# Kernel optimization log

Hardware: AMD Instinct MI355X
Metric: run time of the kernel (lower is better)

Reference implementation:

```python
import jax, jax.numpy as jnp
import numpy as np

HEADS, DIM_HEAD, DIM = 8, 64, 512
INNER = HEADS * DIM_HEAD  # 512


def setup_inputs() -> dict:
    key = jax.random.key(0)
    k1, k2, k3 = jax.random.split(key, 3)
    b, n = 2, 2048
    x = jax.random.normal(k1, (b, n, DIM), dtype=jnp.float32)
    # to_qkv: Linear(dim, 4*inner_dim, bias=False); weight stored [out, in]
    w_qkv = jax.random.normal(k2, (4 * INNER, DIM), dtype=jnp.float32) * (1.0 / np.sqrt(DIM))
    # to_out: Linear(2*inner_dim, dim) with bias
    w_out = jax.random.normal(k3, (DIM, 2 * INNER), dtype=jnp.float32) * (1.0 / np.sqrt(2 * INNER))
    b_out = jnp.zeros((DIM,), dtype=jnp.float32)
    return {"x": x, "w_qkv": w_qkv, "w_out": w_out, "b_out": b_out}


def reference(x, w_qkv, w_out, b_out):
    b, n, d = x.shape
    qkvt = x @ w_qkv.T  # [b, n, 4*inner]
    q, k, v, t = jnp.split(qkvt, 4, axis=-1)

    def split_heads(z):
        return z.reshape(b, n, HEADS, DIM_HEAD).transpose(0, 2, 1, 3)  # [b,h,n,dh]

    q, k, v, t = map(split_heads, (q, k, v, t))

    scale = DIM_HEAD ** -0.5
    dots = jnp.einsum('bhid,bhjd->bhij', q, k) * scale
    attn1 = jax.nn.softmax(dots, axis=-1)

    # fixed positional-decay attention: exp(-|i-j|/e), torch broadcast-normalized
    idx = jnp.arange(1, n + 1, dtype=x.dtype)  # linspace(1, n, n)
    tg = jnp.abs(idx[None, :] - idx[:, None])  # [n, n]
    a2 = jnp.exp(-tg / jnp.exp(jnp.asarray(1.0, x.dtype)))
    a2 = a2 / a2.sum(-1)  # broadcasts over last axis, as in the torch code

    out1 = jnp.einsum('bhij,bhjd->bhid', attn1, v)
    out2 = jnp.einsum('ij,bhjd->bhid', a2, t)
    out = jnp.concatenate([out1, out2], axis=-1)  # [b,h,n,2*dh]
    out = out.transpose(0, 2, 1, 3).reshape(b, n, HEADS * 2 * DIM_HEAD)  # [b,n,2*inner]
    return out @ w_out.T + b_out
```

## Files before the change

### kernel.cpp

```cpp
#include <hip/hip_runtime.h>
#include <stdint.h>

typedef unsigned short u16;
typedef __bf16 bf16;
typedef __bf16 bf16x8 __attribute__((ext_vector_type(8)));
typedef float f32x4 __attribute__((ext_vector_type(4)));

#define NSEQ 2048
#define NDH 64
#define NH 8
#define QKS 2097152ull

__device__ __forceinline__ float b2f(u16 u) {
  union { float f; uint32_t i; } x; x.i = ((uint32_t)u) << 16; return x.f;
}
__device__ __forceinline__ u16 f2b(float f) {
  union { float f; uint32_t i; } x; x.f = f;
  const uint32_t r = x.i + 0x7FFFu + ((x.i >> 16) & 1u);
  return (u16)(r >> 16);
}

__global__ __launch_bounds__(256) void k_cvt(
    const float* __restrict__ x, const float* __restrict__ wqkv,
    const float* __restrict__ wout, u16* __restrict__ xbf,
    u16* __restrict__ wqkvbf, u16* __restrict__ woutbf) {
  const int i = blockIdx.x * 256 + threadIdx.x;
  const float* src; u16* dst; int off;
  if (i < 524288)      { src = x;    dst = xbf;    off = i; }
  else if (i < 786432) { src = wqkv; dst = wqkvbf; off = i - 524288; }
  else                 { src = wout; dst = woutbf; off = i - 786432; }
  const float4 v = *(const float4*)(src + (size_t)off * 4);
  u16 t[4] = {f2b(v.x), f2b(v.y), f2b(v.z), f2b(v.w)};
  *(uint2*)(dst + (size_t)off * 4) = *(const uint2*)t;
}

__global__ __launch_bounds__(256) void k_gemm_qkvt(
    const u16* __restrict__ X, const u16* __restrict__ W, u16* __restrict__ qkvt) {
  __shared__ __align__(16) bf16 smem[18432];
  bf16* As = smem;
  bf16* Bs = smem + 5120;
  const int tid = threadIdx.x;
  const int n0 = blockIdx.x * 128;
  const int m0 = blockIdx.y * 128;
  const int w = tid >> 6, lane = tid & 63;
  const int wy = w >> 1, wx = w & 1;
  const int quad = lane >> 4, l15 = lane & 15;
  const int srow = tid >> 1, shalf = (tid & 1) * 16;
  const u16* ax = X + (size_t)(m0 + srow) * 512 + shalf;
  const u16* bx = W + (size_t)(n0 + srow) * 512 + shalf;
  f32x4 acc[4][4];
#pragma unroll
  for (int mt = 0; mt < 4; ++mt)
#pragma unroll
    for (int nt = 0; nt < 4; ++nt) acc[mt][nt] = (f32x4){0.f, 0.f, 0.f, 0.f};
  uint4 a0 = *(const uint4*)ax, a1 = *(const uint4*)(ax + 8);
  uint4 b0 = *(const uint4*)bx, b1 = *(const uint4*)(bx + 8);
  for (int kc = 0; kc < 512; kc += 32) {
    __syncthreads();
    *(uint4*)&As[srow * 40 + shalf]     = a0;
    *(uint4*)&As[srow * 40 + shalf + 8] = a1;
    *(uint4*)&Bs[srow * 40 + shalf]     = b0;
    *(uint4*)&Bs[srow * 40 + shalf + 8] = b1;
    __syncthreads();
    if (kc + 32 < 512) {
      a0 = *(const uint4*)(ax + kc + 32);
      a1 = *(const uint4*)(ax + kc + 40);
      b0 = *(const uint4*)(bx + kc + 32);
      b1 = *(const uint4*)(bx + kc + 40);
    }
    bf16x8 af[4], bfr[4];
#pragma unroll
    for (int mt = 0; mt < 4; ++mt)
      af[mt] = *(const bf16x8*)&As[(wy * 64 + mt * 16 + l15) * 40 + quad * 8];
#pragma unroll
    for (int nt = 0; nt < 4; ++nt)
      bfr[nt] = *(const bf16x8*)&Bs[(wx * 64 + nt * 16 + l15) * 40 + quad * 8];
#pragma unroll
    for (int mt = 0; mt < 4; ++mt)
#pragma unroll
      for (int nt = 0; nt < 4; ++nt)
        acc[mt][nt] = __builtin_amdgcn_mfma_f32_16x16x32_bf16(af[mt], bfr[nt], acc[mt][nt], 0, 0, 0);
  }
  __syncthreads();
  const int cbase = n0 + wx * 64;
  const int which = cbase >> 9;
  const int h     = (cbase >> 6) & 7;
  const float scale = (which == 0) ? 0.18033688011112043f : 1.0f;
  bf16* Cw = smem + w * 4608;
  if (which == 2) {
#pragma unroll
    for (int nt = 0; nt < 4; ++nt)
#pragma unroll
      for (int mt = 0; mt < 4; ++mt)
#pragma unroll
        for (int r = 0; r < 4; ++r)
          Cw[(nt * 16 + l15) * 72 + mt * 16 + quad * 4 + r] = (bf16)acc[mt][nt][r];
  } else {
#pragma unroll
    for (int mt = 0; mt < 4; ++mt)
#pragma unroll
      for (int nt = 0; nt < 4; ++nt)
#pragma unroll
        for (int r = 0; r < 4; ++r)
          Cw[(mt * 16 + quad * 4 + r) * 72 + nt * 16 + l15] = (bf16)(acc[mt][nt][r] * scale);
  }
  const int mb = m0 + wy * 64;
  const int bb = mb >> 11;
  const int nn0 = mb & (NSEQ - 1);
  if (which == 2) {
    u16* vt = qkvt + 2ull * QKS + (size_t)(bb * NH + h) * NDH * NSEQ;
#pragma unroll
    for (int p = 0; p < 8; ++p) {
      const int d = p * 8 + (lane >> 3);
      const int t8 = (lane & 7) * 8;
      const uint4 v = *(const uint4*)&Cw[d * 72 + t8];
      *(uint4*)(vt + (size_t)d * NSEQ + nn0 + t8) = v;
    }
  } else {
    u16* dst = qkvt + (size_t)which * QKS + ((size_t)(bb * NH + h) * NSEQ + nn0) * NDH;
#pragma unroll
    for (int p = 0; p < 8; ++p) {
      const int tok = p * 8 + (lane >> 3);
      const int c8 = (lane & 7) * 8;
      const uint4 v = *(const uint4*)&Cw[tok * 72 + c8];
      *(uint4*)(dst + (size_t)tok * NDH + c8) = v;
    }
  }
}

__global__ __launch_bounds__(256) void k_attn(
    const u16* __restrict__ qkvt, u16* __restrict__ out12) {
  __shared__ __align__(16) bf16 Qs[64][72];
  __shared__ __align__(16) bf16 Ks[64][72];
  __shared__ __align__(16) bf16 Vt[64][72];
  __shared__ __align__(16) bf16 Pw[64][72];
  const int tid = threadIdx.x;
  const int q0  = blockIdx.x * 64;
  const int bh  = blockIdx.y;
  const size_t base  = (size_t)bh * (NSEQ * NDH);
  const size_t vbase = 2ull * QKS + (size_t)bh * (NDH * NSEQ);
  const int wq = tid >> 6, lane = tid & 63;
  const int quad = lane >> 4, l15 = lane & 15;
  const int srow = tid >> 2, sc0 = (tid & 3) * 16;
  {
    const u16* qp = qkvt + base + (size_t)(q0 + srow) * NDH + sc0;
    *(uint4*)&Qs[srow][sc0]     = *(const uint4*)qp;
    *(uint4*)&Qs[srow][sc0 + 8] = *(const uint4*)(qp + 8);
  }
  __syncthreads();
  const bf16x8 qa0 = *(const bf16x8*)&Qs[wq * 16 + l15][quad * 8];
  const bf16x8 qa1 = *(const bf16x8*)&Qs[wq * 16 + l15][32 + quad * 8];
  bf16x8 vones;
#pragma unroll
  for (int j = 0; j < 8; ++j) vones[j] = (l15 == 0) ? (bf16)1.f : (bf16)0.f;
  f32x4 lacc = {0.f, 0.f, 0.f, 0.f};
  f32x4 o[4] = {{0.f,0.f,0.f,0.f},{0.f,0.f,0.f,0.f},{0.f,0.f,0.f,0.f},{0.f,0.f,0.f,0.f}};
  const u16* kp = qkvt + QKS + base + (size_t)srow * NDH + sc0;
  const u16* vp = qkvt + vbase + (size_t)srow * NSEQ + sc0;
  uint4 k0 = *(const uint4*)kp;
  uint4 k1 = *(const uint4*)(kp + 8);
  uint4 v0 = *(const uint4*)vp;
  uint4 v1 = *(const uint4*)(vp + 8);
  for (int kt = 0; kt < 32; ++kt) {
    __syncthreads();
    *(uint4*)&Ks[srow][sc0]     = k0;
    *(uint4*)&Ks[srow][sc0 + 8] = k1;
    *(uint4*)&Vt[srow][sc0]     = v0;
    *(uint4*)&Vt[srow][sc0 + 8] = v1;
    __syncthreads();
    if (kt < 31) {
      const u16* kn = kp + (size_t)(kt + 1) * 64 * NDH;
      const u16* vn = vp + (kt + 1) * 64;
      k0 = *(const uint4*)kn;
      k1 = *(const uint4*)(kn + 8);
      v0 = *(const uint4*)vn;
      v1 = *(const uint4*)(vn + 8);
    }
    f32x4 s[4] = {{0.f,0.f,0.f,0.f},{0.f,0.f,0.f,0.f},{0.f,0.f,0.f,0.f},{0.f,0.f,0.f,0.f}};
#pragma unroll
    for (int t = 0; t < 4; ++t) {
      const bf16x8 kb0 = *(const bf16x8*)&Ks[t * 16 + l15][quad * 8];
      const bf16x8 kb1 = *(const bf16x8*)&Ks[t * 16 + l15][32 + quad * 8];
      s[t] = __builtin_amdgcn_mfma_f32_16x16x32_bf16(qa0, kb0, s[t], 0, 0, 0);
      s[t] = __builtin_amdgcn_mfma_f32_16x16x32_bf16(qa1, kb1, s[t], 0, 0, 0);
    }
#pragma unroll
    for (int r = 0; r < 4; ++r) {
      const int prow = wq * 16 + quad * 4 + r;
      Pw[prow][l15]      = (bf16)__builtin_amdgcn_exp2f(s[0][r]);
      Pw[prow][16 + l15] = (bf16)__builtin_amdgcn_exp2f(s[1][r]);
      Pw[prow][32 + l15] = (bf16)__builtin_amdgcn_exp2f(s[2][r]);
      Pw[prow][48 + l15] = (bf16)__builtin_amdgcn_exp2f(s[3][r]);
    }
#pragma unroll
    for (int c = 0; c < 2; ++c) {
      const bf16x8 pa = *(const bf16x8*)&Pw[wq * 16 + l15][c * 32 + quad * 8];
      lacc = __builtin_amdgcn_mfma_f32_16x16x32_bf16(pa, vones, lacc, 0, 0, 0);
#pragma unroll
      for (int nt = 0; nt < 4; ++nt) {
        const bf16x8 vb = *(const bf16x8*)&Vt[nt * 16 + l15][c * 32 + quad * 8];
        o[nt] = __builtin_amdgcn_mfma_f32_16x16x32_bf16(pa, vb, o[nt], 0, 0, 0);
      }
    }
  }
  const int bb = bh >> 3, h = bh & 7;
#pragma unroll
  for (int r = 0; r < 4; ++r) {
    const float lsum = __shfl(lacc[r], lane & 48);
    const float inv = 1.f / lsum;
    const int nn = q0 + wq * 16 + quad * 4 + r;
    u16* dst = out12 + (size_t)(bb * NSEQ + nn) * 1024 + h * 128;
#pragma unroll
    for (int nt = 0; nt < 4; ++nt)
      dst[nt * 16 + l15] = f2b(o[nt][r] * inv);
  }
}

__global__ __launch_bounds__(256) void k_band(
    const u16* __restrict__ qkvt, u16* __restrict__ out12) {
  __shared__ float sinv[4][192];
  __shared__ float fbuf[4][64][68];
  const int tid = threadIdx.x;
  const int w = tid >> 6, d = tid & 63;
  const int c  = blockIdx.x * 4 + w;
  const int i0 = c * 64;
  const int bh = blockIdx.y;
  const size_t tb = 3ull * QKS + (size_t)bh * (NSEQ * NDH);
  const float EI = 0.36787944117144233f;
  const float RR = 0.69220062755534635f;
  const float OMR = 1.f - RR;
#pragma unroll
  for (int p = 0; p < 3; ++p) {
    const int j = i0 - 64 + p * 64 + d;
    const float r1 = __expf(-(float)(j + 1) * EI);
    const float r2 = __expf(-(float)(NSEQ - j) * EI);
    sinv[w][p * 64 + d] = OMR / (1.f - r1 + RR - r2);
  }
  const u16* tp = qkvt + tb + d;
  float f = 0.f;
  if (c > 0) {
#pragma unroll 8
    for (int jj = 0; jj < 64; ++jj)
      f = RR * f + sinv[w][jj] * b2f(tp[(size_t)(i0 - 64 + jj) * NDH]);
  }
#pragma unroll 8
  for (int jj = 0; jj < 64; ++jj) {
    f = RR * f + sinv[w][64 + jj] * b2f(tp[(size_t)(i0 + jj) * NDH]);
    fbuf[w][jj][d] = f;
  }
  float b = 0.f;
  if (c < 31) {
#pragma unroll 8
    for (int jj = 63; jj >= 0; --jj)
      b = RR * b + sinv[w][128 + jj] * b2f(tp[(size_t)(i0 + 64 + jj) * NDH]);
  }
  const int bb = bh >> 3, h = bh & 7;
#pragma unroll 8
  for (int jj = 63; jj >= 0; --jj) {
    const float g = sinv[w][64 + jj] * b2f(tp[(size_t)(i0 + jj) * NDH]);
    b = RR * b + g;
    out12[(size_t)(bb * NSEQ + i0 + jj) * 1024 + h * 128 + 64 + d] =
        f2b(fbuf[w][jj][d] + b - g);
  }
}

__global__ __launch_bounds__(256) void k_gemm_out(
    const u16* __restrict__ A, const u16* __restrict__ W,
    const float* __restrict__ bias, float* __restrict__ out) {
  __shared__ __align__(16) float smemf[8704];
  bf16* As = (bf16*)smemf;
  bf16* Bs = (bf16*)smemf + 5120;
  const int tid = threadIdx.x;
  const int n0 = blockIdx.x * 64;
  const int m0 = blockIdx.y * 128;
  const int w = tid >> 6, lane = tid & 63;
  const int quad = lane >> 4, l15 = lane & 15;
  const int srow = tid >> 1, shalf = (tid & 1) * 16;
  const u16* ap = A + (size_t)(m0 + srow) * 1024 + shalf;
  const int brow = (tid & 127) >> 1;
  const u16* bp = W + (size_t)(n0 + brow) * 1024 + shalf;
  f32x4 acc[2][4];
#pragma unroll
  for (int mt = 0; mt < 2; ++mt)
#pragma unroll
    for (int nt = 0; nt < 4; ++nt) acc[mt][nt] = (f32x4){0.f, 0.f, 0.f, 0.f};
  uint4 a0 = *(const uint4*)ap, a1 = *(const uint4*)(ap + 8);
  uint4 b0 = {}, b1 = {};
  if (tid < 128) { b0 = *(const uint4*)bp; b1 = *(const uint4*)(bp + 8); }
  for (int kc = 0; kc < 1024; kc += 32) {
    __syncthreads();
    *(uint4*)&As[srow * 40 + shalf]     = a0;
    *(uint4*)&As[srow * 40 + shalf + 8] = a1;
    if (tid < 128) {
      *(uint4*)&Bs[brow * 40 + shalf]     = b0;
      *(uint4*)&Bs[brow * 40 + shalf + 8] = b1;
    }
    __syncthreads();
    if (kc + 32 < 1024) {
      a0 = *(const uint4*)(ap + kc + 32);
      a1 = *(const uint4*)(ap + kc + 40);
      if (tid < 128) {
        b0 = *(const uint4*)(bp + kc + 32);
        b1 = *(const uint4*)(bp + kc + 40);
      }
    }
    bf16x8 af[2], bfr[4];
#pragma unroll
    for (int mt = 0; mt < 2; ++mt)
      af[mt] = *(const bf16x8*)&As[(w * 32 + mt * 16 + l15) * 40 + quad * 8];
#pragma unroll
    for (int nt = 0; nt < 4; ++nt)
      bfr[nt] = *(const bf16x8*)&Bs[(nt * 16 + l15) * 40 + quad * 8];
#pragma unroll
    for (int mt = 0; mt < 2; ++mt)
#pragma unroll
      for (int nt = 0; nt < 4; ++nt)
        acc[mt][nt] = __builtin_amdgcn_mfma_f32_16x16x32_bf16(af[mt], bfr[nt], acc[mt][nt], 0, 0, 0);
  }
  float bias_v[4];
#pragma unroll
  for (int nt = 0; nt < 4; ++nt) bias_v[nt] = bias[n0 + nt * 16 + l15];
  __syncthreads();
  float* Cw = smemf + w * 2176;
#pragma unroll
  for (int mt = 0; mt < 2; ++mt)
#pragma unroll
    for (int nt = 0; nt < 4; ++nt)
#pragma unroll
      for (int r = 0; r < 4; ++r)
        Cw[(mt * 16 + quad * 4 + r) * 68 + nt * 16 + l15] = acc[mt][nt][r] + bias_v[nt];
#pragma unroll
  for (int p = 0; p < 8; ++p) {
    const int row = p * 4 + (lane >> 4);
    const int c4  = lane & 15;
    const float4 v = *(const float4*)&Cw[row * 68 + c4 * 4];
    *(float4*)(out + (size_t)(m0 + w * 32 + row) * 512 + n0 + c4 * 4) = v;
  }
}

extern "C" void kernel_launch(void* const* d_in, const int* in_sizes, int n_in,
                              void* d_out, int out_size, void* d_ws, size_t ws_size,
                              hipStream_t stream) {
  (void)in_sizes; (void)n_in; (void)out_size; (void)ws_size;
  const float* x     = (const float*)d_in[0];
  const float* w_qkv = (const float*)d_in[1];
  const float* w_out = (const float*)d_in[2];
  const float* b_out = (const float*)d_in[3];
  float* out = (float*)d_out;
  u16* qkvt    = (u16*)d_ws;
  u16* out12   = (u16*)d_ws + 8ull * 1024 * 1024;
  u16* xbf     = out12;
  u16* wqkvbf  = (u16*)d_ws + 10ull * 1024 * 1024;
  u16* woutbf  = (u16*)d_ws + 12ull * 1024 * 1024;
  k_cvt      <<<3584, 256, 0, stream>>>(x, w_qkv, w_out, xbf, wqkvbf, woutbf);
  k_gemm_qkvt<<<dim3(16, 32), 256, 0, stream>>>(xbf, wqkvbf, qkvt);
  k_attn     <<<dim3(32, 16), 256, 0, stream>>>(qkvt, out12);
  k_band     <<<dim3(8, 16), 256, 0, stream>>>(qkvt, out12);
  k_gemm_out <<<dim3(8, 32), 256, 0, stream>>>(out12, woutbf, b_out, out);
}
```

Before: 158.1 us.

## Process 128 query rows per attention block to reuse K/V tiles

Each attention block now handles 128 queries instead of 64, with every wave owning 32 rows, so each K/V tile loaded into shared memory feeds twice as many MFMAs. The grid is halved to 256 blocks and reordered so blockIdx.x indexes batch-head. The P buffer row stride is padded to 76 to change the LDS bank pattern. This cuts global and LDS traffic per query, at the cost of more registers per thread and fewer blocks to spread across the GPU's compute units.

```diff
diff --git a/kernel.cpp b/kernel.cpp
--- a/kernel.cpp
+++ b/kernel.cpp
@@ -130,13 +130,13 @@
 
 __global__ __launch_bounds__(256) void k_attn(
     const u16* __restrict__ qkvt, u16* __restrict__ out12) {
-  __shared__ __align__(16) bf16 Qs[64][72];
+  __shared__ __align__(16) bf16 Qs[128][72];
   __shared__ __align__(16) bf16 Ks[64][72];
   __shared__ __align__(16) bf16 Vt[64][72];
-  __shared__ __align__(16) bf16 Pw[64][72];
+  __shared__ __align__(16) bf16 Pw[128][76];
   const int tid = threadIdx.x;
-  const int q0  = blockIdx.x * 64;
-  const int bh  = blockIdx.y;
+  const int bh  = blockIdx.x;
+  const int q0  = blockIdx.y * 128;
   const size_t base  = (size_t)bh * (NSEQ * NDH);
   const size_t vbase = 2ull * QKS + (size_t)bh * (NDH * NSEQ);
   const int wq = tid >> 6, lane = tid & 63;
@@ -146,15 +146,26 @@
     const u16* qp = qkvt + base + (size_t)(q0 + srow) * NDH + sc0;
     *(uint4*)&Qs[srow][sc0]     = *(const uint4*)qp;
     *(uint4*)&Qs[srow][sc0 + 8] = *(const uint4*)(qp + 8);
+    const u16* qp2 = qp + 64 * NDH;
+    *(uint4*)&Qs[64 + srow][sc0]     = *(const uint4*)qp2;
+    *(uint4*)&Qs[64 + srow][sc0 + 8] = *(const uint4*)(qp2 + 8);
   }
   __syncthreads();
-  const bf16x8 qa0 = *(const bf16x8*)&Qs[wq * 16 + l15][quad * 8];
-  const bf16x8 qa1 = *(const bf16x8*)&Qs[wq * 16 + l15][32 + quad * 8];
+  bf16x8 qa[2][2];
+#pragma unroll
+  for (int i = 0; i < 2; ++i)
+#pragma unroll
+    for (int c = 0; c < 2; ++c)
+      qa[i][c] = *(const bf16x8*)&Qs[wq * 32 + i * 16 + l15][c * 32 + quad * 8];
   bf16x8 vones;
 #pragma unroll
   for (int j = 0; j < 8; ++j) vones[j] = (l15 == 0) ? (bf16)1.f : (bf16)0.f;
-  f32x4 lacc = {0.f, 0.f, 0.f, 0.f};
-  f32x4 o[4] = {{0.f,0.f,0.f,0.f},{0.f,0.f,0.f,0.f},{0.f,0.f,0.f,0.f},{0.f,0.f,0.f,0.f}};
+  f32x4 lacc[2] = {{0.f,0.f,0.f,0.f},{0.f,0.f,0.f,0.f}};
+  f32x4 o[2][4];
+#pragma unroll
+  for (int i = 0; i < 2; ++i)
+#pragma unroll
+    for (int nt = 0; nt < 4; ++nt) o[i][nt] = (f32x4){0.f,0.f,0.f,0.f};
   const u16* kp = qkvt + QKS + base + (size_t)srow * NDH + sc0;
   const u16* vp = qkvt + vbase + (size_t)srow * NSEQ + sc0;
   uint4 k0 = *(const uint4*)kp;
@@ -176,44 +187,61 @@
       v0 = *(const uint4*)vn;
       v1 = *(const uint4*)(vn + 8);
     }
-    f32x4 s[4] = {{0.f,0.f,0.f,0.f},{0.f,0.f,0.f,0.f},{0.f,0.f,0.f,0.f},{0.f,0.f,0.f,0.f}};
+    f32x4 s[2][4];
+#pragma unroll
+    for (int i = 0; i < 2; ++i)
+#pragma unroll
+      for (int t = 0; t < 4; ++t) s[i][t] = (f32x4){0.f,0.f,0.f,0.f};
 #pragma unroll
     for (int t = 0; t < 4; ++t) {
       const bf16x8 kb0 = *(const bf16x8*)&Ks[t * 16 + l15][quad * 8];
       const bf16x8 kb1 = *(const bf16x8*)&Ks[t * 16 + l15][32 + quad * 8];
-      s[t] = __builtin_amdgcn_mfma_f32_16x16x32_bf16(qa0, kb0, s[t], 0, 0, 0);
-      s[t] = __builtin_amdgcn_mfma_f32_16x16x32_bf16(qa1, kb1, s[t], 0, 0, 0);
-    }
-#pragma unroll
-    for (int r = 0; r < 4; ++r) {
-      const int prow = wq * 16 + quad * 4 + r;
-      Pw[prow][l15]      = (bf16)__builtin_amdgcn_exp2f(s[0][r]);
-      Pw[prow][16 + l15] = (bf16)__builtin_amdgcn_exp2f(s[1][r]);
-      Pw[prow][32 + l15] = (bf16)__builtin_amdgcn_exp2f(s[2][r]);
-      Pw[prow][48 + l15] = (bf16)__builtin_amdgcn_exp2f(s[3][r]);
-    }
+#pragma unroll
+      for (int i = 0; i < 2; ++i) {
+        s[i][t] = __builtin_amdgcn_mfma_f32_16x16x32_bf16(qa[i][0], kb0, s[i][t], 0, 0, 0);
+        s[i][t] = __builtin_amdgcn_mfma_f32_16x16x32_bf16(qa[i][1], kb1, s[i][t], 0, 0, 0);
+      }
+    }
+#pragma unroll
+    for (int i = 0; i < 2; ++i)
+#pragma unroll
+      for (int r = 0; r < 4; ++r) {
+        const int prow = wq * 32 + i * 16 + quad * 4 + r;
+        Pw[prow][l15]      = (bf16)__builtin_amdgcn_exp2f(s[i][0][r]);
+        Pw[prow][16 + l15] = (bf16)__builtin_amdgcn_exp2f(s[i][1][r]);
+        Pw[prow][32 + l15] = (bf16)__builtin_amdgcn_exp2f(s[i][2][r]);
+        Pw[prow][48 + l15] = (bf16)__builtin_amdgcn_exp2f(s[i][3][r]);
+      }
 #pragma unroll
     for (int c = 0; c < 2; ++c) {
-      const bf16x8 pa = *(const bf16x8*)&Pw[wq * 16 + l15][c * 32 + quad * 8];
-      lacc = __builtin_amdgcn_mfma_f32_16x16x32_bf16(pa, vones, lacc, 0, 0, 0);
+      bf16x8 pa[2];
+#pragma unroll
+      for (int i = 0; i < 2; ++i) {
+        pa[i] = *(const bf16x8*)&Pw[wq * 32 + i * 16 + l15][c * 32 + quad * 8];
+        lacc[i] = __builtin_amdgcn_mfma_f32_16x16x32_bf16(pa[i], vones, lacc[i], 0, 0, 0);
+      }
 #pragma unroll
       for (int nt = 0; nt < 4; ++nt) {
         const bf16x8 vb = *(const bf16x8*)&Vt[nt * 16 + l15][c * 32 + quad * 8];
-        o[nt] = __builtin_amdgcn_mfma_f32_16x16x32_bf16(pa, vb, o[nt], 0, 0, 0);
+#pragma unroll
+        for (int i = 0; i < 2; ++i)
+          o[i][nt] = __builtin_amdgcn_mfma_f32_16x16x32_bf16(pa[i], vb, o[i][nt], 0, 0, 0);
       }
     }
   }
   const int bb = bh >> 3, h = bh & 7;
 #pragma unroll
-  for (int r = 0; r < 4; ++r) {
-    const float lsum = __shfl(lacc[r], lane & 48);
-    const float inv = 1.f / lsum;
-    const int nn = q0 + wq * 16 + quad * 4 + r;
-    u16* dst = out12 + (size_t)(bb * NSEQ + nn) * 1024 + h * 128;
-#pragma unroll
-    for (int nt = 0; nt < 4; ++nt)
-      dst[nt * 16 + l15] = f2b(o[nt][r] * inv);
-  }
+  for (int i = 0; i < 2; ++i)
+#pragma unroll
+    for (int r = 0; r < 4; ++r) {
+      const float lsum = __shfl(lacc[i][r], lane & 48);
+      const float inv = 1.f / lsum;
+      const int nn = q0 + wq * 32 + i * 16 + quad * 4 + r;
+      u16* dst = out12 + (size_t)(bb * NSEQ + nn) * 1024 + h * 128;
+#pragma unroll
+      for (int nt = 0; nt < 4; ++nt)
+        dst[nt * 16 + l15] = f2b(o[i][nt][r] * inv);
+    }
 }
 
 __global__ __launch_bounds__(256) void k_band(
@@ -354,7 +382,7 @@
   u16* woutbf  = (u16*)d_ws + 12ull * 1024 * 1024;
   k_cvt      <<<3584, 256, 0, stream>>>(x, w_qkv, w_out, xbf, wqkvbf, woutbf);
   k_gemm_qkvt<<<dim3(16, 32), 256, 0, stream>>>(xbf, wqkvbf, qkvt);
-  k_attn     <<<dim3(32, 16), 256, 0, stream>>>(qkvt, out12);
+  k_attn     <<<dim3(16, 16), 256, 0, stream>>>(qkvt, out12);
   k_band     <<<dim3(8, 16), 256, 0, stream>>>(qkvt, out12);
   k_gemm_out <<<dim3(8, 32), 256, 0, stream>>>(out12, woutbf, b_out, out);
 }
```

Result: slower. 163.5 us (+3.4%).

## Fuse fp32-to-bf16 conversion into GEMM loads and retile output GEMM

Applied to the files above, without the earlier changes.

Removes the standalone conversion kernel: the QKV and output GEMMs now read fp32 inputs and weights directly and convert to bf16 while staging into shared memory. This saves one launch and a round trip of bf16 copies through memory, but the GEMMs now read twice the bytes and redo the weight conversion in every block. The output GEMM moves to 64x64 tiles, doubling the block count. The attention grid swaps its axes so consecutive blocks share a head, and the P tile row stride is padded from 72 to 76.

```diff
diff --git a/kernel.cpp b/kernel.cpp
--- a/kernel.cpp
+++ b/kernel.cpp
@@ -20,22 +20,8 @@
   return (u16)(r >> 16);
 }
 
-__global__ __launch_bounds__(256) void k_cvt(
-    const float* __restrict__ x, const float* __restrict__ wqkv,
-    const float* __restrict__ wout, u16* __restrict__ xbf,
-    u16* __restrict__ wqkvbf, u16* __restrict__ woutbf) {
-  const int i = blockIdx.x * 256 + threadIdx.x;
-  const float* src; u16* dst; int off;
-  if (i < 524288)      { src = x;    dst = xbf;    off = i; }
-  else if (i < 786432) { src = wqkv; dst = wqkvbf; off = i - 524288; }
-  else                 { src = wout; dst = woutbf; off = i - 786432; }
-  const float4 v = *(const float4*)(src + (size_t)off * 4);
-  u16 t[4] = {f2b(v.x), f2b(v.y), f2b(v.z), f2b(v.w)};
-  *(uint2*)(dst + (size_t)off * 4) = *(const uint2*)t;
-}
-
 __global__ __launch_bounds__(256) void k_gemm_qkvt(
-    const u16* __restrict__ X, const u16* __restrict__ W, u16* __restrict__ qkvt) {
+    const float* __restrict__ X, const float* __restrict__ W, u16* __restrict__ qkvt) {
   __shared__ __align__(16) bf16 smem[18432];
   bf16* As = smem;
   bf16* Bs = smem + 5120;
@@ -46,32 +32,47 @@
   const int wy = w >> 1, wx = w & 1;
   const int quad = lane >> 4, l15 = lane & 15;
   const int srow = tid >> 1, shalf = (tid & 1) * 16;
-  const u16* ax = X + (size_t)(m0 + srow) * 512 + shalf;
-  const u16* bx = W + (size_t)(n0 + srow) * 512 + shalf;
+  const float* ax = X + (size_t)(m0 + srow) * 512 + shalf;
+  const float* bx = W + (size_t)(n0 + srow) * 512 + shalf;
   f32x4 acc[4][4];
 #pragma unroll
   for (int mt = 0; mt < 4; ++mt)
 #pragma unroll
     for (int nt = 0; nt < 4; ++nt) acc[mt][nt] = (f32x4){0.f, 0.f, 0.f, 0.f};
-  uint4 a0 = *(const uint4*)ax, a1 = *(const uint4*)(ax + 8);
-  uint4 b0 = *(const uint4*)bx, b1 = *(const uint4*)(bx + 8);
+  float4 af[4], bf4[4];
+#pragma unroll
+  for (int p = 0; p < 4; ++p) {
+    af[p]  = *(const float4*)(ax + p * 4);
+    bf4[p] = *(const float4*)(bx + p * 4);
+  }
   for (int kc = 0; kc < 512; kc += 32) {
     __syncthreads();
-    *(uint4*)&As[srow * 40 + shalf]     = a0;
-    *(uint4*)&As[srow * 40 + shalf + 8] = a1;
-    *(uint4*)&Bs[srow * 40 + shalf]     = b0;
-    *(uint4*)&Bs[srow * 40 + shalf + 8] = b1;
+    {
+      u16 ta[8] = {f2b(af[0].x), f2b(af[0].y), f2b(af[0].z), f2b(af[0].w),
+                   f2b(af[1].x), f2b(af[1].y), f2b(af[1].z), f2b(af[1].w)};
+      u16 tb[8] = {f2b(af[2].x), f2b(af[2].y), f2b(af[2].z), f2b(af[2].w),
+                   f2b(af[3].x), f2b(af[3].y), f2b(af[3].z), f2b(af[3].w)};
+      *(uint4*)&As[srow * 40 + shalf]     = *(const uint4*)ta;
+      *(uint4*)&As[srow * 40 + shalf + 8] = *(const uint4*)tb;
+      u16 tc[8] = {f2b(bf4[0].x), f2b(bf4[0].y), f2b(bf4[0].z), f2b(bf4[0].w),
+                   f2b(bf4[1].x), f2b(bf4[1].y), f2b(bf4[1].z), f2b(bf4[1].w)};
+      u16 td[8] = {f2b(bf4[2].x), f2b(bf4[2].y), f2b(bf4[2].z), f2b(bf4[2].w),
+                   f2b(bf4[3].x), f2b(bf4[3].y), f2b(bf4[3].z), f2b(bf4[3].w)};
+      *(uint4*)&Bs[srow * 40 + shalf]     = *(const uint4*)tc;
+      *(uint4*)&Bs[srow * 40 + shalf + 8] = *(const uint4*)td;
+    }
     __syncthreads();
     if (kc + 32 < 512) {
-      a0 = *(const uint4*)(ax + kc + 32);
-      a1 = *(const uint4*)(ax + kc + 40);
-      b0 = *(const uint4*)(bx + kc + 32);
-      b1 = *(const uint4*)(bx + kc + 40);
-    }
-    bf16x8 af[4], bfr[4];
+#pragma unroll
+      for (int p = 0; p < 4; ++p) {
+        af[p]  = *(const float4*)(ax + kc + 32 + p * 4);
+        bf4[p] = *(const float4*)(bx + kc + 32 + p * 4);
+      }
+    }
+    bf16x8 afr[4], bfr[4];
 #pragma unroll
     for (int mt = 0; mt < 4; ++mt)
-      af[mt] = *(const bf16x8*)&As[(wy * 64 + mt * 16 + l15) * 40 + quad * 8];
+      afr[mt] = *(const bf16x8*)&As[(wy * 64 + mt * 16 + l15) * 40 + quad * 8];
 #pragma unroll
     for (int nt = 0; nt < 4; ++nt)
       bfr[nt] = *(const bf16x8*)&Bs[(wx * 64 + nt * 16 + l15) * 40 + quad * 8];
@@ -79,7 +80,7 @@
     for (int mt = 0; mt < 4; ++mt)
 #pragma unroll
       for (int nt = 0; nt < 4; ++nt)
-        acc[mt][nt] = __builtin_amdgcn_mfma_f32_16x16x32_bf16(af[mt], bfr[nt], acc[mt][nt], 0, 0, 0);
+        acc[mt][nt] = __builtin_amdgcn_mfma_f32_16x16x32_bf16(afr[mt], bfr[nt], acc[mt][nt], 0, 0, 0);
   }
   __syncthreads();
   const int cbase = n0 + wx * 64;
@@ -133,10 +134,10 @@
   __shared__ __align__(16) bf16 Qs[64][72];
   __shared__ __align__(16) bf16 Ks[64][72];
   __shared__ __align__(16) bf16 Vt[64][72];
-  __shared__ __align__(16) bf16 Pw[64][72];
+  __shared__ __align__(16) bf16 Pw[64][76];
   const int tid = threadIdx.x;
-  const int q0  = blockIdx.x * 64;
-  const int bh  = blockIdx.y;
+  const int bh  = blockIdx.x;
+  const int q0  = blockIdx.y * 64;
   const size_t base  = (size_t)bh * (NSEQ * NDH);
   const size_t vbase = 2ull * QKS + (size_t)bh * (NDH * NSEQ);
   const int wq = tid >> 6, lane = tid & 63;
@@ -265,76 +266,62 @@
 }
 
 __global__ __launch_bounds__(256) void k_gemm_out(
-    const u16* __restrict__ A, const u16* __restrict__ W,
+    const u16* __restrict__ A, const float* __restrict__ W,
     const float* __restrict__ bias, float* __restrict__ out) {
-  __shared__ __align__(16) float smemf[8704];
+  __shared__ __align__(16) float smemf[4352];
   bf16* As = (bf16*)smemf;
-  bf16* Bs = (bf16*)smemf + 5120;
+  bf16* Bs = (bf16*)smemf + 2560;
   const int tid = threadIdx.x;
   const int n0 = blockIdx.x * 64;
-  const int m0 = blockIdx.y * 128;
+  const int m0 = blockIdx.y * 64;
   const int w = tid >> 6, lane = tid & 63;
   const int quad = lane >> 4, l15 = lane & 15;
-  const int srow = tid >> 1, shalf = (tid & 1) * 16;
-  const u16* ap = A + (size_t)(m0 + srow) * 1024 + shalf;
-  const int brow = (tid & 127) >> 1;
-  const u16* bp = W + (size_t)(n0 + brow) * 1024 + shalf;
-  f32x4 acc[2][4];
-#pragma unroll
-  for (int mt = 0; mt < 2; ++mt)
-#pragma unroll
-    for (int nt = 0; nt < 4; ++nt) acc[mt][nt] = (f32x4){0.f, 0.f, 0.f, 0.f};
-  uint4 a0 = *(const uint4*)ap, a1 = *(const uint4*)(ap + 8);
-  uint4 b0 = {}, b1 = {};
-  if (tid < 128) { b0 = *(const uint4*)bp; b1 = *(const uint4*)(bp + 8); }
+  const int srow = tid >> 2, scol = (tid & 3) * 8;
+  const u16*   ap = A + (size_t)(m0 + srow) * 1024 + scol;
+  const float* bp = W + (size_t)(n0 + srow) * 1024 + scol;
+  f32x4 acc[4];
+#pragma unroll
+  for (int nt = 0; nt < 4; ++nt) acc[nt] = (f32x4){0.f, 0.f, 0.f, 0.f};
+  uint4 a0 = *(const uint4*)ap;
+  float4 b0 = *(const float4*)bp;
+  float4 b1 = *(const float4*)(bp + 4);
   for (int kc = 0; kc < 1024; kc += 32) {
     __syncthreads();
-    *(uint4*)&As[srow * 40 + shalf]     = a0;
-    *(uint4*)&As[srow * 40 + shalf + 8] = a1;
-    if (tid < 128) {
-      *(uint4*)&Bs[brow * 40 + shalf]     = b0;
-      *(uint4*)&Bs[brow * 40 + shalf + 8] = b1;
+    *(uint4*)&As[srow * 40 + scol] = a0;
+    {
+      u16 tb[8] = {f2b(b0.x), f2b(b0.y), f2b(b0.z), f2b(b0.w),
+                   f2b(b1.x), f2b(b1.y), f2b(b1.z), f2b(b1.w)};
+      *(uint4*)&Bs[srow * 40 + scol] = *(const uint4*)tb;
     }
     __syncthreads();
     if (kc + 32 < 1024) {
       a0 = *(const uint4*)(ap + kc + 32);
-      a1 = *(const uint4*)(ap + kc + 40);
-      if (tid < 128) {
-        b0 = *(const uint4*)(bp + kc + 32);
-        b1 = *(const uint4*)(bp + kc + 40);
-      }
-    }
-    bf16x8 af[2], bfr[4];
-#pragma unroll
-    for (int mt = 0; mt < 2; ++mt)
-      af[mt] = *(const bf16x8*)&As[(w * 32 + mt * 16 + l15) * 40 + quad * 8];
-#pragma unroll
-    for (int nt = 0; nt < 4; ++nt)
-      bfr[nt] = *(const bf16x8*)&Bs[(nt * 16 + l15) * 40 + quad * 8];
-#pragma unroll
-    for (int mt = 0; mt < 2; ++mt)
-#pragma unroll
-      for (int nt = 0; nt < 4; ++nt)
-        acc[mt][nt] = __builtin_amdgcn_mfma_f32_16x16x32_bf16(af[mt], bfr[nt], acc[mt][nt], 0, 0, 0);
+      b0 = *(const float4*)(bp + kc + 32);
+      b1 = *(const float4*)(bp + kc + 36);
+    }
+    const bf16x8 af = *(const bf16x8*)&As[(w * 16 + l15) * 40 + quad * 8];
+#pragma unroll
+    for (int nt = 0; nt < 4; ++nt) {
+      const bf16x8 bfr = *(const bf16x8*)&Bs[(nt * 16 + l15) * 40 + quad * 8];
+      acc[nt] = __builtin_amdgcn_mfma_f32_16x16x32_bf16(af, bfr, acc[nt], 0, 0, 0);
+    }
   }
   float bias_v[4];
 #pragma unroll
   for (int nt = 0; nt < 4; ++nt) bias_v[nt] = bias[n0 + nt * 16 + l15];
   __syncthreads();
-  float* Cw = smemf + w * 2176;
-#pragma unroll
-  for (int mt = 0; mt < 2; ++mt)
-#pragma unroll
-    for (int nt = 0; nt < 4; ++nt)
-#pragma unroll
-      for (int r = 0; r < 4; ++r)
-        Cw[(mt * 16 + quad * 4 + r) * 68 + nt * 16 + l15] = acc[mt][nt][r] + bias_v[nt];
-#pragma unroll
-  for (int p = 0; p < 8; ++p) {
+  float* Cw = smemf + w * 1088;
+#pragma unroll
+  for (int nt = 0; nt < 4; ++nt)
+#pragma unroll
+    for (int r = 0; r < 4; ++r)
+      Cw[(quad * 4 + r) * 68 + nt * 16 + l15] = acc[nt][r] + bias_v[nt];
+#pragma unroll
+  for (int p = 0; p < 4; ++p) {
     const int row = p * 4 + (lane >> 4);
-    const int c4  = lane & 15;
-    const float4 v = *(const float4*)&Cw[row * 68 + c4 * 4];
-    *(float4*)(out + (size_t)(m0 + w * 32 + row) * 512 + n0 + c4 * 4) = v;
+    const int c4  = (lane & 15) * 4;
+    const float4 v = *(const float4*)&Cw[row * 68 + c4];
+    *(float4*)(out + (size_t)(m0 + w * 16 + row) * 512 + n0 + c4) = v;
   }
 }
 
@@ -347,14 +334,10 @@
   const float* w_out = (const float*)d_in[2];
   const float* b_out = (const float*)d_in[3];
   float* out = (float*)d_out;
-  u16* qkvt    = (u16*)d_ws;
-  u16* out12   = (u16*)d_ws + 8ull * 1024 * 1024;
-  u16* xbf     = out12;
-  u16* wqkvbf  = (u16*)d_ws + 10ull * 1024 * 1024;
-  u16* woutbf  = (u16*)d_ws + 12ull * 1024 * 1024;
-  k_cvt      <<<3584, 256, 0, stream>>>(x, w_qkv, w_out, xbf, wqkvbf, woutbf);
-  k_gemm_qkvt<<<dim3(16, 32), 256, 0, stream>>>(xbf, wqkvbf, qkvt);
-  k_attn     <<<dim3(32, 16), 256, 0, stream>>>(qkvt, out12);
+  u16* qkvt  = (u16*)d_ws;
+  u16* out12 = (u16*)d_ws + 8ull * 1024 * 1024;
+  k_gemm_qkvt<<<dim3(16, 32), 256, 0, stream>>>(x, w_qkv, qkvt);
+  k_attn     <<<dim3(16, 32), 256, 0, stream>>>(qkvt, out12);
   k_band     <<<dim3(8, 16), 256, 0, stream>>>(qkvt, out12);
-  k_gemm_out <<<dim3(8, 32), 256, 0, stream>>>(out12, woutbf, b_out, out);
-}
+  k_gemm_out <<<dim3(8, 64), 256, 0, stream>>>(out12, w_out, b_out, out);
+}
```

Result: no change. 160.4 us (+1.5%).
